# Performance work log

Hardware: AMD Instinct MI355X
Metric: run time of the kernel (lower is better)

Reference implementation:

```python
import jax, jax.numpy as jnp
import numpy as np

B, S, HID = 2, 2048, 2048
NH = 16
QLR, KVLR = 1536, 512
DN, DR, DV = 128, 64, 128          # qk_nope_head_dim, qk_rope_head_dim, v_head_dim
DQK = DN + DR                      # 192
SCALE = DQK ** -0.5
EPS = 1e-6


def rmsnorm(x, w):
    return x * jax.lax.rsqrt(jnp.mean(x * x, axis=-1, keepdims=True) + EPS) * w


def rotate_half(x):
    h = x.shape[-1] // 2
    return jnp.concatenate([-x[..., h:], x[..., :h]], axis=-1)


def setup_inputs() -> dict:
    key = jax.random.key(0)
    k = jax.random.split(key, 8)
    hidden_states = jax.random.normal(k[0], (B, S, HID), jnp.float32)
    # additive causal mask [B,1,S,S]
    causal = jnp.tril(jnp.ones((S, S), bool))
    attention_mask = jnp.where(causal, 0.0, -1e9).astype(jnp.float32)[None, None]
    attention_mask = jnp.broadcast_to(attention_mask, (B, 1, S, S))
    # RoPE tables for the rope head dim
    inv_freq = 1.0 / (10000.0 ** (jnp.arange(0, DR, 2, dtype=jnp.float32) / DR))
    t = jnp.arange(S, dtype=jnp.float32)[:, None] * inv_freq[None, :]
    emb = jnp.concatenate([t, t], axis=-1)        # [S, DR]
    cos, sin = jnp.cos(emb), jnp.sin(emb)
    s = 0.02
    w_qa = jax.random.normal(k[1], (HID, QLR), jnp.float32) * s
    qa_ln = jnp.ones((QLR,), jnp.float32)
    w_qb = jax.random.normal(k[2], (QLR, NH * DQK), jnp.float32) * s
    w_kva = jax.random.normal(k[3], (HID, KVLR + DR), jnp.float32) * s
    kva_ln = jnp.ones((KVLR,), jnp.float32)
    w_kvb = jax.random.normal(k[4], (KVLR, NH * (DN + DV)), jnp.float32) * s
    w_o = jax.random.normal(k[5], (NH * DV, HID), jnp.float32) * s
    return {"hidden_states": hidden_states, "attention_mask": attention_mask,
            "cos": cos, "sin": sin, "w_qa": w_qa, "qa_ln": qa_ln, "w_qb": w_qb,
            "w_kva": w_kva, "kva_ln": kva_ln, "w_kvb": w_kvb, "w_o": w_o}


def reference(hidden_states, attention_mask, cos, sin, w_qa, qa_ln, w_qb,
              w_kva, kva_ln, w_kvb, w_o):
    b, s, _ = hidden_states.shape
    # q low-rank path: q_b_proj(q_a_layernorm(q_a_proj(x)))
    q = rmsnorm(hidden_states @ w_qa, qa_ln) @ w_qb            # [B,S,NH*DQK]
    q = q.reshape(b, s, NH, DQK).transpose(0, 2, 1, 3)          # [B,NH,S,DQK]
    q_nope, q_pe = q[..., :DN], q[..., DN:]
    # compressed kv + shared rope key
    ckv = hidden_states @ w_kva                                 # [B,S,KVLR+DR]
    k_c, k_pe = ckv[..., :KVLR], ckv[..., KVLR:]
    kv = rmsnorm(k_c, kva_ln) @ w_kvb                           # [B,S,NH*(DN+DV)]
    kv = kv.reshape(b, s, NH, DN + DV).transpose(0, 2, 1, 3)    # [B,NH,S,DN+DV]
    k_nope, value_states = kv[..., :DN], kv[..., DN:]
    # RoPE on rope dims (k_pe is MQA: one head)
    k_pe = k_pe.reshape(b, 1, s, DR)
    c = cos[None, None]  # [1,1,S,DR]
    si = sin[None, None]
    q_pe = q_pe * c + rotate_half(q_pe) * si
    k_pe = k_pe * c + rotate_half(k_pe) * si
    k_pe = jnp.broadcast_to(k_pe, (b, NH, s, DR))
    query_states = jnp.concatenate([q_nope, q_pe], axis=-1)     # [B,NH,S,DQK]
    key_states = jnp.concatenate([k_nope, k_pe], axis=-1)       # [B,NH,S,DQK]
    attn_weights = jnp.einsum('bhqd,bhkd->bhqk', query_states, key_states) * SCALE
    attn_weights = attn_weights + attention_mask
    attn_probs = jax.nn.softmax(attn_weights.astype(jnp.float32), axis=-1)
    attn_probs = attn_probs.astype(value_states.dtype)
    attn_output = jnp.einsum('bhqk,bhkd->bhqd', attn_probs, value_states)
    attn_output = attn_output.transpose(0, 2, 1, 3).reshape(b, s, NH * DV)
    return attn_output @ w_o                                    # [B,S,HID]
```

## Files before the change

kernel.cpp:

```cpp
#include <hip/hip_runtime.h>
#include <type_traits>

typedef __attribute__((ext_vector_type(8))) short  vshort8;
typedef __attribute__((ext_vector_type(8))) __bf16 vbf16x8;
typedef __attribute__((ext_vector_type(4))) float  vfloat4;

__device__ __forceinline__ float bf2f(unsigned short h) {
    return __uint_as_float(((unsigned int)h) << 16);
}
__device__ __forceinline__ unsigned short f2bf(float f) {
    unsigned int u = __float_as_uint(f);
    unsigned int r = (u + 0x7FFFu + ((u >> 16) & 1u)) >> 16;
    return (unsigned short)r;
}
__device__ __forceinline__ vshort8 cvt8s(const float* p, float s) {
    float4 a = *(const float4*)p;
    float4 b = *(const float4*)(p + 4);
    vshort8 r;
    r[0] = (short)f2bf(a.x * s); r[1] = (short)f2bf(a.y * s);
    r[2] = (short)f2bf(a.z * s); r[3] = (short)f2bf(a.w * s);
    r[4] = (short)f2bf(b.x * s); r[5] = (short)f2bf(b.y * s);
    r[6] = (short)f2bf(b.z * s); r[7] = (short)f2bf(b.w * s);
    return r;
}
__device__ __forceinline__ vshort8 cvt8(const float* p) { return cvt8s(p, 1.0f); }
__device__ __forceinline__ void gload16(const void* g, void* lds) {
    __builtin_amdgcn_global_load_lds(
        (const __attribute__((address_space(1))) unsigned int*)g,
        (__attribute__((address_space(3))) unsigned int*)lds, 16, 0, 0);
}

__global__ __launch_bounds__(256) void hconv_kernel(
    const float* __restrict__ in, unsigned short* __restrict__ out, int n8)
{
    int i = blockIdx.x * 256 + threadIdx.x;
    if (i < n8) *(vshort8*)(out + (size_t)i * 8) = cvt8(in + (size_t)i * 8);
}

__global__ __launch_bounds__(256) void wtrans_kernel(
    const float* __restrict__ W, unsigned short* __restrict__ Wt,
    int ldw, int ldt, int rowoff, float scale)
{
    __shared__ __align__(16) unsigned short Ls[64][72];
    const int t = threadIdx.x;
    const int n0 = blockIdx.x * 64, k0 = blockIdx.y * 64;
    const int rr = t >> 2, cc = t & 3;

    const float* src = W + (size_t)(k0 + rr) * ldw + n0 + cc * 16;
    *(vshort8*)&Ls[rr][cc * 16]     = cvt8s(src, scale);
    *(vshort8*)&Ls[rr][cc * 16 + 8] = cvt8s(src + 8, scale);
    __syncthreads();

    unsigned short* dst = Wt + (size_t)(rowoff + n0 + rr) * ldt + k0 + cc * 16;
    vshort8 v0, v1;
    #pragma unroll
    for (int j = 0; j < 8; ++j) {
        v0[j] = (short)Ls[cc * 16 + j][rr];
        v1[j] = (short)Ls[cc * 16 + 8 + j][rr];
    }
    *(vshort8*)dst = v0;
    *(vshort8*)(dst + 8) = v1;
}

template<typename CT>
__global__ __launch_bounds__(256) void gemm_tt(
    const unsigned short* __restrict__ A, const unsigned short* __restrict__ Bt,
    CT* __restrict__ C0, CT* __restrict__ C1,
    int K, int N, int nsplit, int ldc0, int ldc1)
{
    __shared__ __align__(16) unsigned short As[128 * 32];
    __shared__ __align__(16) unsigned short Bs[128 * 32];

    const int t = threadIdx.x, lane = t & 63, w = t >> 6;
    const int lm = lane & 15, quad = lane >> 4;
    const int wm = w >> 1, wn = w & 1;
    const int m0 = blockIdx.y * 128, n0 = blockIdx.x * 128;
    const int srow = lane >> 2, sseg = lane & 3;

    vfloat4 acc[4][4] = {};

    for (int k0 = 0; k0 < K; k0 += 32) {
        #pragma unroll
        for (int j = 0; j < 2; ++j) {
            int r = w * 32 + j * 16 + srow;
            gload16(A  + (size_t)(m0 + r) * K + k0 + sseg * 8, &As[(w * 2 + j) * 512]);
            gload16(Bt + (size_t)(n0 + r) * K + k0 + sseg * 8, &Bs[(w * 2 + j) * 512]);
        }
        __syncthreads();

        vbf16x8 af[4], bw[4];
        #pragma unroll
        for (int i = 0; i < 4; ++i) {
            af[i] = *(const vbf16x8*)&As[(wm * 64 + i * 16 + lm) * 32 + quad * 8];
            bw[i] = *(const vbf16x8*)&Bs[(wn * 64 + i * 16 + lm) * 32 + quad * 8];
        }
        #pragma unroll
        for (int mi = 0; mi < 4; ++mi)
            #pragma unroll
            for (int ni = 0; ni < 4; ++ni)
                acc[mi][ni] = __builtin_amdgcn_mfma_f32_16x16x32_bf16(af[mi], bw[ni], acc[mi][ni], 0, 0, 0);
        __syncthreads();
    }

    #pragma unroll
    for (int mi = 0; mi < 4; ++mi) {
        #pragma unroll
        for (int ni = 0; ni < 4; ++ni) {
            int col = n0 + wn * 64 + ni * 16 + lm;
            if (col >= N) continue;
            #pragma unroll
            for (int r = 0; r < 4; ++r) {
                int row = m0 + wm * 64 + mi * 16 + quad * 4 + r;
                float v = acc[mi][ni][r];
                if (col < nsplit) {
                    if constexpr (std::is_same_v<CT, float>) C0[(size_t)row * ldc0 + col] = v;
                    else C0[(size_t)row * ldc0 + col] = f2bf(v);
                } else {
                    if constexpr (std::is_same_v<CT, float>) C1[(size_t)row * ldc1 + col - nsplit] = v;
                    else C1[(size_t)row * ldc1 + col - nsplit] = f2bf(v);
                }
            }
        }
    }
}

__global__ __launch_bounds__(256) void gemm_kv(
    const unsigned short* __restrict__ A, const unsigned short* __restrict__ Bt,
    unsigned short* __restrict__ Kn, unsigned short* __restrict__ VT, int K)
{
    __shared__ __align__(16) unsigned short As[128 * 32];
    __shared__ __align__(16) unsigned short Bs[128 * 32];

    const int t = threadIdx.x, lane = t & 63, w = t >> 6;
    const int lm = lane & 15, quad = lane >> 4;
    const int wm = w >> 1, wn = w & 1;
    const int m0 = blockIdx.y * 128, n0 = blockIdx.x * 128;
    const int srow = lane >> 2, sseg = lane & 3;

    vfloat4 acc[4][4] = {};

    for (int k0 = 0; k0 < K; k0 += 32) {
        #pragma unroll
        for (int j = 0; j < 2; ++j) {
            int r = w * 32 + j * 16 + srow;
            gload16(A  + (size_t)(m0 + r) * K + k0 + sseg * 8, &As[(w * 2 + j) * 512]);
            gload16(Bt + (size_t)(n0 + r) * K + k0 + sseg * 8, &Bs[(w * 2 + j) * 512]);
        }
        __syncthreads();

        vbf16x8 af[4], bw[4];
        #pragma unroll
        for (int i = 0; i < 4; ++i) {
            af[i] = *(const vbf16x8*)&As[(wm * 64 + i * 16 + lm) * 32 + quad * 8];
            bw[i] = *(const vbf16x8*)&Bs[(wn * 64 + i * 16 + lm) * 32 + quad * 8];
        }
        #pragma unroll
        for (int mi = 0; mi < 4; ++mi)
            #pragma unroll
            for (int ni = 0; ni < 4; ++ni)
                acc[mi][ni] = __builtin_amdgcn_mfma_f32_16x16x32_bf16(af[mi], bw[ni], acc[mi][ni], 0, 0, 0);
        __syncthreads();
    }

    #pragma unroll
    for (int mi = 0; mi < 4; ++mi) {
        #pragma unroll
        for (int ni = 0; ni < 4; ++ni) {
            int col = n0 + wn * 64 + ni * 16 + lm;
            int h = col >> 8, d = col & 255;
            #pragma unroll
            for (int r = 0; r < 4; ++r) {
                int row = m0 + wm * 64 + mi * 16 + quad * 4 + r;
                float v = acc[mi][ni][r];
                if (d < 128) {
                    Kn[(size_t)row * 2048 + h * 128 + d] = f2bf(v);
                } else {
                    int b = row >> 11, tok = row & 2047;
                    VT[((size_t)(b * 16 + h) * 128 + d - 128) * 2048 + tok] = f2bf(v);
                }
            }
        }
    }
}

__global__ __launch_bounds__(256) void rmsnorm_kernel(
    const unsigned short* __restrict__ in, const float* __restrict__ wgt,
    unsigned short* __restrict__ out, int width, int ld_in, int ld_out)
{
    const int row = blockIdx.x;
    const int t = threadIdx.x;
    const unsigned short* x = in + (size_t)row * ld_in;

    float ss = 0.f;
    for (int i = t; i < width; i += 256) { float v = bf2f(x[i]); ss += v * v; }
    #pragma unroll
    for (int off = 32; off > 0; off >>= 1) ss += __shfl_down(ss, off, 64);

    __shared__ float red[4];
    __shared__ float rr;
    if ((t & 63) == 0) red[t >> 6] = ss;
    __syncthreads();
    if (t == 0) rr = rsqrtf((red[0] + red[1] + red[2] + red[3]) / (float)width + 1e-6f);
    __syncthreads();
    float r = rr;
    unsigned short* o = out + (size_t)row * ld_out;
    for (int i = t; i < width; i += 256) o[i] = f2bf(bf2f(x[i]) * r * wgt[i]);
}

__global__ __launch_bounds__(256) void rope_q_kernel(
    unsigned short* __restrict__ q, const float* __restrict__ cosb,
    const float* __restrict__ sinb)
{
    const int row = blockIdx.x;
    const int s = row & 2047;
    const int t = threadIdx.x;
    unsigned short* qr = q + (size_t)row * 3072;
    const int i = t & 31;
    const float cs = cosb[s * 64 + i];
    const float sn = sinb[s * 64 + i];

    #pragma unroll
    for (int c = t; c < 512; c += 256) {
        int h = c >> 5;
        unsigned short* p = qr + h * 192 + 128 + i;
        float x = bf2f(p[0]);
        float y = bf2f(p[32]);
        p[0]  = f2bf(x * cs - y * sn);
        p[32] = f2bf(y * cs + x * sn);
    }
}

__global__ __launch_bounds__(64) void rope_k_kernel(
    const unsigned short* __restrict__ ckv, const float* __restrict__ cosb,
    const float* __restrict__ sinb, unsigned short* __restrict__ kpe)
{
    const int row = blockIdx.x;
    const int s = row & 2047;
    const int t = threadIdx.x;
    if (t < 32) {
        float cs = cosb[s * 64 + t];
        float sn = sinb[s * 64 + t];
        float x = bf2f(ckv[(size_t)row * 576 + 512 + t]);
        float y = bf2f(ckv[(size_t)row * 576 + 544 + t]);
        kpe[(size_t)row * 64 + t]      = f2bf(x * cs - y * sn);
        kpe[(size_t)row * 64 + 32 + t] = f2bf(y * cs + x * sn);
    }
}

__global__ __launch_bounds__(256) void flash_kernel(
    const unsigned short* __restrict__ Q, const unsigned short* __restrict__ Kn,
    const unsigned short* __restrict__ KPE, const unsigned short* __restrict__ VT,
    unsigned short* __restrict__ O)
{
    __shared__ __align__(16) unsigned short Ks[64][200];
    __shared__ __align__(16) unsigned short Vs[128][72];
    __shared__ __align__(16) unsigned short Ps[4][16][72];

    const int t    = threadIdx.x;
    const int lane = t & 63;
    const int w    = t >> 6;
    const int lm   = lane & 15, quad = lane >> 4;
    const int h = blockIdx.y, b = blockIdx.z;
    const int tb = b * 2048;
    const unsigned short* VTbh = VT + (size_t)(b * 16 + h) * 128 * 2048;

    for (int pi = 0; pi < 2; ++pi) {
        const int qt = pi ? (31 - blockIdx.x) : blockIdx.x;

        const int qtok = tb + qt * 64 + w * 16 + lm;
        vbf16x8 aq[6];
        #pragma unroll
        for (int ch = 0; ch < 6; ++ch)
            aq[ch] = *(const vbf16x8*)(Q + (size_t)qtok * 3072 + h * 192 + ch * 32 + quad * 8);

        vfloat4 acc_o[8];
        #pragma unroll
        for (int i = 0; i < 8; ++i) acc_o[i] = (vfloat4){0, 0, 0, 0};
        float mrow[4], lrow[4];
        #pragma unroll
        for (int r = 0; r < 4; ++r) { mrow[r] = -3.0e38f; lrow[r] = 0.f; }

        for (int kt = 0; kt <= qt; ++kt) {
            const int kb = kt * 64;
            #pragma unroll
            for (int it = 0; it < 4; ++it) {
                int idx = t + it * 256;
                int row = idx >> 4, sg = idx & 15;
                *(vshort8*)&Ks[row][sg * 8] =
                    *(const vshort8*)(Kn + (size_t)(tb + kb + row) * 2048 + h * 128 + sg * 8);
            }
            #pragma unroll
            for (int it = 0; it < 2; ++it) {
                int idx = t + it * 256;
                int row = idx >> 3, sg = idx & 7;
                *(vshort8*)&Ks[row][128 + sg * 8] =
                    *(const vshort8*)(KPE + (size_t)(tb + kb + row) * 64 + sg * 8);
            }
            #pragma unroll
            for (int it = 0; it < 4; ++it) {
                int idx = t + it * 256;
                int d = idx >> 3, sg = idx & 7;
                *(vshort8*)&Vs[d][sg * 8] =
                    *(const vshort8*)(VTbh + (size_t)d * 2048 + kb + sg * 8);
            }
            __syncthreads();

            vfloat4 accs[4];
            #pragma unroll
            for (int ni = 0; ni < 4; ++ni) accs[ni] = (vfloat4){0, 0, 0, 0};
            #pragma unroll
            for (int ni = 0; ni < 4; ++ni) {
                #pragma unroll
                for (int ch = 0; ch < 6; ++ch) {
                    vbf16x8 bk = *(const vbf16x8*)&Ks[ni * 16 + lm][ch * 32 + quad * 8];
                    accs[ni] = __builtin_amdgcn_mfma_f32_16x16x32_bf16(aq[ch], bk, accs[ni], 0, 0, 0);
                }
            }

            const int qrow = qt * 64 + w * 16 + quad * 4;
            #pragma unroll
            for (int ni = 0; ni < 4; ++ni) {
                int ki = kb + ni * 16 + lm;
                #pragma unroll
                for (int r = 0; r < 4; ++r)
                    if (ki > qrow + r) accs[ni][r] = -3.0e38f;
            }

            #pragma unroll
            for (int r = 0; r < 4; ++r) {
                float mx = fmaxf(fmaxf(accs[0][r], accs[1][r]), fmaxf(accs[2][r], accs[3][r]));
                #pragma unroll
                for (int off = 1; off < 16; off <<= 1) mx = fmaxf(mx, __shfl_xor(mx, off, 64));
                float mnew  = fmaxf(mrow[r], mx);
                float alpha = __expf(mrow[r] - mnew);
                float sum = 0.f;
                #pragma unroll
                for (int ni = 0; ni < 4; ++ni) {
                    float pv = __expf(accs[ni][r] - mnew);
                    accs[ni][r] = pv;
                    sum += pv;
                }
                #pragma unroll
                for (int off = 1; off < 16; off <<= 1) sum += __shfl_xor(sum, off, 64);
                lrow[r] = lrow[r] * alpha + sum;
                mrow[r] = mnew;
                #pragma unroll
                for (int vt = 0; vt < 8; ++vt) acc_o[vt][r] *= alpha;
            }

            #pragma unroll
            for (int ni = 0; ni < 4; ++ni)
                #pragma unroll
                for (int r = 0; r < 4; ++r)
                    Ps[w][quad * 4 + r][ni * 16 + lm] = f2bf(accs[ni][r]);
            __syncthreads();

            #pragma unroll
            for (int kc = 0; kc < 2; ++kc) {
                vbf16x8 ap = *(const vbf16x8*)&Ps[w][lm][kc * 32 + quad * 8];
                #pragma unroll
                for (int vt = 0; vt < 8; ++vt) {
                    vbf16x8 bv = *(const vbf16x8*)&Vs[vt * 16 + lm][kc * 32 + quad * 8];
                    acc_o[vt] = __builtin_amdgcn_mfma_f32_16x16x32_bf16(ap, bv, acc_o[vt], 0, 0, 0);
                }
            }
            __syncthreads();
        }

        #pragma unroll
        for (int r = 0; r < 4; ++r) {
            float inv = 1.f / lrow[r];
            int tok = tb + qt * 64 + w * 16 + quad * 4 + r;
            #pragma unroll
            for (int vt = 0; vt < 8; ++vt)
                O[(size_t)tok * 2048 + h * 128 + vt * 16 + lm] = f2bf(acc_o[vt][r] * inv);
        }
    }
}

extern "C" void kernel_launch(void* const* d_in, const int* in_sizes, int n_in,
                              void* d_out, int out_size, void* d_ws, size_t ws_size,
                              hipStream_t stream) {
    const float* hidden = (const float*)d_in[0];
    const float* cosb   = (const float*)d_in[2];
    const float* sinb   = (const float*)d_in[3];
    const float* w_qa   = (const float*)d_in[4];
    const float* qa_ln  = (const float*)d_in[5];
    const float* w_qb   = (const float*)d_in[6];
    const float* w_kva  = (const float*)d_in[7];
    const float* kva_ln = (const float*)d_in[8];
    const float* w_kvb  = (const float*)d_in[9];
    const float* w_o    = (const float*)d_in[10];
    float* out = (float*)d_out;
    const float SCALE = 0.07216878364870323f;

    unsigned short* ws   = (unsigned short*)d_ws;
    unsigned short* hb   = ws;
    unsigned short* Kn   = ws;
    unsigned short* wt12 = ws + 8388608;
    unsigned short* VT   = ws + 8388608;
    unsigned short* ot   = ws + 8388608;
    unsigned short* qbuf = ws + 16777216;
    unsigned short* q_a  = ws + 29360128;
    unsigned short* ckv  = ws + 35651584;
    unsigned short* aout = ws + 29360128;
    unsigned short* qbt  = ws + 38010880;
    unsigned short* kvbt = ws + 42729472;
    unsigned short* kvn  = ws + 44826624;
    unsigned short* kpe  = ws + 46923776;

    dim3 blk(256);

    hconv_kernel<<<4096, blk, 0, stream>>>(hidden, hb, 1048576);
    wtrans_kernel<<<dim3(24, 32), blk, 0, stream>>>(w_qa,  wt12, 1536, 2048, 0,    1.0f);
    wtrans_kernel<<<dim3( 9, 32), blk, 0, stream>>>(w_kva, wt12,  576, 2048, 1536, 1.0f);
    wtrans_kernel<<<dim3(48, 24), blk, 0, stream>>>(w_qb,  qbt,  3072, 1536, 0,    SCALE);
    wtrans_kernel<<<dim3(64,  8), blk, 0, stream>>>(w_kvb, kvbt, 4096,  512, 0,    1.0f);

    gemm_tt<unsigned short><<<dim3(17, 32), blk, 0, stream>>>(
        hb, wt12, q_a, ckv, 2048, 2112, 1536, 1536, 576);

    rmsnorm_kernel<<<4096, blk, 0, stream>>>(q_a, qa_ln, q_a, 1536, 1536, 1536);
    rmsnorm_kernel<<<4096, blk, 0, stream>>>(ckv, kva_ln, kvn, 512, 576, 512);
    rope_k_kernel<<<4096, dim3(64), 0, stream>>>(ckv, cosb, sinb, kpe);

    gemm_tt<unsigned short><<<dim3(24, 32), blk, 0, stream>>>(
        q_a, qbt, qbuf, qbuf, 1536, 3072, 3072, 3072, 3072);
    rope_q_kernel<<<4096, blk, 0, stream>>>(qbuf, cosb, sinb);

    gemm_kv<<<dim3(32, 32), blk, 0, stream>>>(kvn, kvbt, Kn, VT, 512);

    flash_kernel<<<dim3(16, 16, 2), blk, 0, stream>>>(qbuf, Kn, kpe, VT, aout);

    wtrans_kernel<<<dim3(32, 32), blk, 0, stream>>>(w_o, ot, 2048, 2048, 0, 1.0f);

    gemm_tt<float><<<dim3(16, 32), blk, 0, stream>>>(
        aout, ot, out, out, 2048, 2048, 2048, 2048, 2048);
}
```

Measured before the change: 546.1 us.

## Stage V transpose through LDS in gemm_kv and give flash one q-tile per block

The gemm_kv epilogue now splits by block column parity. K blocks write Kn directly, and V blocks stage their tile transposed in shared memory so that VT is written with coalesced 16-byte stores instead of scattered 2-byte writes. The flash kernel no longer pairs q-tiles inside each block. It launches 32x16x2 blocks, one q-tile each, ordered heaviest first, which doubles the number of blocks for better occupancy and gives up the explicit load balance of pairing. The extra shared-memory tile and barriers in gemm_kv add a little epilogue cost.

```diff
diff --git a/kernel.cpp b/kernel.cpp
--- a/kernel.cpp
+++ b/kernel.cpp
@@ -130,6 +130,7 @@
 {
     __shared__ __align__(16) unsigned short As[128 * 32];
     __shared__ __align__(16) unsigned short Bs[128 * 32];
+    __shared__ __align__(16) unsigned short Ts[64][136];
 
     const int t = threadIdx.x, lane = t & 63, w = t >> 6;
     const int lm = lane & 15, quad = lane >> 4;
@@ -162,23 +163,51 @@
         __syncthreads();
     }
 
-    #pragma unroll
-    for (int mi = 0; mi < 4; ++mi) {
-        #pragma unroll
-        for (int ni = 0; ni < 4; ++ni) {
-            int col = n0 + wn * 64 + ni * 16 + lm;
-            int h = col >> 8, d = col & 255;
-            #pragma unroll
-            for (int r = 0; r < 4; ++r) {
-                int row = m0 + wm * 64 + mi * 16 + quad * 4 + r;
-                float v = acc[mi][ni][r];
-                if (d < 128) {
-                    Kn[(size_t)row * 2048 + h * 128 + d] = f2bf(v);
-                } else {
-                    int b = row >> 11, tok = row & 2047;
-                    VT[((size_t)(b * 16 + h) * 128 + d - 128) * 2048 + tok] = f2bf(v);
+    if (!(blockIdx.x & 1)) {
+        const int hh = blockIdx.x >> 1;
+        #pragma unroll
+        for (int mi = 0; mi < 4; ++mi) {
+            #pragma unroll
+            for (int ni = 0; ni < 4; ++ni) {
+                int d = wn * 64 + ni * 16 + lm;
+                #pragma unroll
+                for (int r = 0; r < 4; ++r) {
+                    int row = m0 + wm * 64 + mi * 16 + quad * 4 + r;
+                    Kn[(size_t)row * 2048 + hh * 128 + d] = f2bf(acc[mi][ni][r]);
                 }
             }
+        }
+    } else {
+        const int hh   = blockIdx.x >> 1;
+        const int bb   = m0 >> 11;
+        const int tok0 = m0 & 2047;
+        #pragma unroll
+        for (int half = 0; half < 2; ++half) {
+            if (wn == half) {
+                #pragma unroll
+                for (int mi = 0; mi < 4; ++mi) {
+                    #pragma unroll
+                    for (int ni = 0; ni < 4; ++ni) {
+                        int ln = ni * 16 + lm;
+                        int rt = wm * 64 + mi * 16 + quad * 4;
+                        #pragma unroll
+                        for (int r = 0; r < 4; ++r)
+                            Ts[ln][rt + r] = f2bf(acc[mi][ni][r]);
+                    }
+                }
+            }
+            __syncthreads();
+            {
+                int tr = t >> 2, seg = t & 3;
+                int dv = half * 64 + tr;
+                unsigned short* dst =
+                    VT + ((size_t)(bb * 16 + hh) * 128 + dv) * 2048 + tok0 + seg * 32;
+                const unsigned short* srcp = &Ts[tr][seg * 32];
+                #pragma unroll
+                for (int j = 0; j < 4; ++j)
+                    *(vshort8*)(dst + j * 8) = *(const vshort8*)(srcp + j * 8);
+            }
+            __syncthreads();
         }
     }
 }
@@ -263,118 +292,115 @@
     const int h = blockIdx.y, b = blockIdx.z;
     const int tb = b * 2048;
     const unsigned short* VTbh = VT + (size_t)(b * 16 + h) * 128 * 2048;
-
-    for (int pi = 0; pi < 2; ++pi) {
-        const int qt = pi ? (31 - blockIdx.x) : blockIdx.x;
-
-        const int qtok = tb + qt * 64 + w * 16 + lm;
-        vbf16x8 aq[6];
-        #pragma unroll
-        for (int ch = 0; ch < 6; ++ch)
-            aq[ch] = *(const vbf16x8*)(Q + (size_t)qtok * 3072 + h * 192 + ch * 32 + quad * 8);
-
-        vfloat4 acc_o[8];
-        #pragma unroll
-        for (int i = 0; i < 8; ++i) acc_o[i] = (vfloat4){0, 0, 0, 0};
-        float mrow[4], lrow[4];
-        #pragma unroll
-        for (int r = 0; r < 4; ++r) { mrow[r] = -3.0e38f; lrow[r] = 0.f; }
-
-        for (int kt = 0; kt <= qt; ++kt) {
-            const int kb = kt * 64;
-            #pragma unroll
-            for (int it = 0; it < 4; ++it) {
-                int idx = t + it * 256;
-                int row = idx >> 4, sg = idx & 15;
-                *(vshort8*)&Ks[row][sg * 8] =
-                    *(const vshort8*)(Kn + (size_t)(tb + kb + row) * 2048 + h * 128 + sg * 8);
-            }
-            #pragma unroll
-            for (int it = 0; it < 2; ++it) {
-                int idx = t + it * 256;
-                int row = idx >> 3, sg = idx & 7;
-                *(vshort8*)&Ks[row][128 + sg * 8] =
-                    *(const vshort8*)(KPE + (size_t)(tb + kb + row) * 64 + sg * 8);
-            }
-            #pragma unroll
-            for (int it = 0; it < 4; ++it) {
-                int idx = t + it * 256;
-                int d = idx >> 3, sg = idx & 7;
-                *(vshort8*)&Vs[d][sg * 8] =
-                    *(const vshort8*)(VTbh + (size_t)d * 2048 + kb + sg * 8);
-            }
-            __syncthreads();
-
-            vfloat4 accs[4];
-            #pragma unroll
-            for (int ni = 0; ni < 4; ++ni) accs[ni] = (vfloat4){0, 0, 0, 0};
+    const int qt = 31 - (int)blockIdx.x;
+
+    const int qtok = tb + qt * 64 + w * 16 + lm;
+    vbf16x8 aq[6];
+    #pragma unroll
+    for (int ch = 0; ch < 6; ++ch)
+        aq[ch] = *(const vbf16x8*)(Q + (size_t)qtok * 3072 + h * 192 + ch * 32 + quad * 8);
+
+    vfloat4 acc_o[8];
+    #pragma unroll
+    for (int i = 0; i < 8; ++i) acc_o[i] = (vfloat4){0, 0, 0, 0};
+    float mrow[4], lrow[4];
+    #pragma unroll
+    for (int r = 0; r < 4; ++r) { mrow[r] = -3.0e38f; lrow[r] = 0.f; }
+
+    for (int kt = 0; kt <= qt; ++kt) {
+        const int kb = kt * 64;
+        #pragma unroll
+        for (int it = 0; it < 4; ++it) {
+            int idx = t + it * 256;
+            int row = idx >> 4, sg = idx & 15;
+            *(vshort8*)&Ks[row][sg * 8] =
+                *(const vshort8*)(Kn + (size_t)(tb + kb + row) * 2048 + h * 128 + sg * 8);
+        }
+        #pragma unroll
+        for (int it = 0; it < 2; ++it) {
+            int idx = t + it * 256;
+            int row = idx >> 3, sg = idx & 7;
+            *(vshort8*)&Ks[row][128 + sg * 8] =
+                *(const vshort8*)(KPE + (size_t)(tb + kb + row) * 64 + sg * 8);
+        }
+        #pragma unroll
+        for (int it = 0; it < 4; ++it) {
+            int idx = t + it * 256;
+            int d = idx >> 3, sg = idx & 7;
+            *(vshort8*)&Vs[d][sg * 8] =
+                *(const vshort8*)(VTbh + (size_t)d * 2048 + kb + sg * 8);
+        }
+        __syncthreads();
+
+        vfloat4 accs[4];
+        #pragma unroll
+        for (int ni = 0; ni < 4; ++ni) accs[ni] = (vfloat4){0, 0, 0, 0};
+        #pragma unroll
+        for (int ni = 0; ni < 4; ++ni) {
+            #pragma unroll
+            for (int ch = 0; ch < 6; ++ch) {
+                vbf16x8 bk = *(const vbf16x8*)&Ks[ni * 16 + lm][ch * 32 + quad * 8];
+                accs[ni] = __builtin_amdgcn_mfma_f32_16x16x32_bf16(aq[ch], bk, accs[ni], 0, 0, 0);
+            }
+        }
+
+        const int qrow = qt * 64 + w * 16 + quad * 4;
+        #pragma unroll
+        for (int ni = 0; ni < 4; ++ni) {
+            int ki = kb + ni * 16 + lm;
+            #pragma unroll
+            for (int r = 0; r < 4; ++r)
+                if (ki > qrow + r) accs[ni][r] = -3.0e38f;
+        }
+
+        #pragma unroll
+        for (int r = 0; r < 4; ++r) {
+            float mx = fmaxf(fmaxf(accs[0][r], accs[1][r]), fmaxf(accs[2][r], accs[3][r]));
+            #pragma unroll
+            for (int off = 1; off < 16; off <<= 1) mx = fmaxf(mx, __shfl_xor(mx, off, 64));
+            float mnew  = fmaxf(mrow[r], mx);
+            float alpha = __expf(mrow[r] - mnew);
+            float sum = 0.f;
             #pragma unroll
             for (int ni = 0; ni < 4; ++ni) {
-                #pragma unroll
-                for (int ch = 0; ch < 6; ++ch) {
-                    vbf16x8 bk = *(const vbf16x8*)&Ks[ni * 16 + lm][ch * 32 + quad * 8];
-                    accs[ni] = __builtin_amdgcn_mfma_f32_16x16x32_bf16(aq[ch], bk, accs[ni], 0, 0, 0);
-                }
-            }
-
-            const int qrow = qt * 64 + w * 16 + quad * 4;
-            #pragma unroll
-            for (int ni = 0; ni < 4; ++ni) {
-                int ki = kb + ni * 16 + lm;
-                #pragma unroll
-                for (int r = 0; r < 4; ++r)
-                    if (ki > qrow + r) accs[ni][r] = -3.0e38f;
-            }
-
-            #pragma unroll
-            for (int r = 0; r < 4; ++r) {
-                float mx = fmaxf(fmaxf(accs[0][r], accs[1][r]), fmaxf(accs[2][r], accs[3][r]));
-                #pragma unroll
-                for (int off = 1; off < 16; off <<= 1) mx = fmaxf(mx, __shfl_xor(mx, off, 64));
-                float mnew  = fmaxf(mrow[r], mx);
-                float alpha = __expf(mrow[r] - mnew);
-                float sum = 0.f;
-                #pragma unroll
-                for (int ni = 0; ni < 4; ++ni) {
-                    float pv = __expf(accs[ni][r] - mnew);
-                    accs[ni][r] = pv;
-                    sum += pv;
-                }
-                #pragma unroll
-                for (int off = 1; off < 16; off <<= 1) sum += __shfl_xor(sum, off, 64);
-                lrow[r] = lrow[r] * alpha + sum;
-                mrow[r] = mnew;
-                #pragma unroll
-                for (int vt = 0; vt < 8; ++vt) acc_o[vt][r] *= alpha;
-            }
-
-            #pragma unroll
-            for (int ni = 0; ni < 4; ++ni)
-                #pragma unroll
-                for (int r = 0; r < 4; ++r)
-                    Ps[w][quad * 4 + r][ni * 16 + lm] = f2bf(accs[ni][r]);
-            __syncthreads();
-
-            #pragma unroll
-            for (int kc = 0; kc < 2; ++kc) {
-                vbf16x8 ap = *(const vbf16x8*)&Ps[w][lm][kc * 32 + quad * 8];
-                #pragma unroll
-                for (int vt = 0; vt < 8; ++vt) {
-                    vbf16x8 bv = *(const vbf16x8*)&Vs[vt * 16 + lm][kc * 32 + quad * 8];
-                    acc_o[vt] = __builtin_amdgcn_mfma_f32_16x16x32_bf16(ap, bv, acc_o[vt], 0, 0, 0);
-                }
-            }
-            __syncthreads();
-        }
-
-        #pragma unroll
-        for (int r = 0; r < 4; ++r) {
-            float inv = 1.f / lrow[r];
-            int tok = tb + qt * 64 + w * 16 + quad * 4 + r;
-            #pragma unroll
-            for (int vt = 0; vt < 8; ++vt)
-                O[(size_t)tok * 2048 + h * 128 + vt * 16 + lm] = f2bf(acc_o[vt][r] * inv);
-        }
+                float pv = __expf(accs[ni][r] - mnew);
+                accs[ni][r] = pv;
+                sum += pv;
+            }
+            #pragma unroll
+            for (int off = 1; off < 16; off <<= 1) sum += __shfl_xor(sum, off, 64);
+            lrow[r] = lrow[r] * alpha + sum;
+            mrow[r] = mnew;
+            #pragma unroll
+            for (int vt = 0; vt < 8; ++vt) acc_o[vt][r] *= alpha;
+        }
+
+        #pragma unroll
+        for (int ni = 0; ni < 4; ++ni)
+            #pragma unroll
+            for (int r = 0; r < 4; ++r)
+                Ps[w][quad * 4 + r][ni * 16 + lm] = f2bf(accs[ni][r]);
+        __syncthreads();
+
+        #pragma unroll
+        for (int kc = 0; kc < 2; ++kc) {
+            vbf16x8 ap = *(const vbf16x8*)&Ps[w][lm][kc * 32 + quad * 8];
+            #pragma unroll
+            for (int vt = 0; vt < 8; ++vt) {
+                vbf16x8 bv = *(const vbf16x8*)&Vs[vt * 16 + lm][kc * 32 + quad * 8];
+                acc_o[vt] = __builtin_amdgcn_mfma_f32_16x16x32_bf16(ap, bv, acc_o[vt], 0, 0, 0);
+            }
+        }
+        __syncthreads();
+    }
+
+    #pragma unroll
+    for (int r = 0; r < 4; ++r) {
+        float inv = 1.f / lrow[r];
+        int tok = tb + qt * 64 + w * 16 + quad * 4 + r;
+        #pragma unroll
+        for (int vt = 0; vt < 8; ++vt)
+            O[(size_t)tok * 2048 + h * 128 + vt * 16 + lm] = f2bf(acc_o[vt][r] * inv);
     }
 }
 
@@ -430,7 +456,7 @@
 
     gemm_kv<<<dim3(32, 32), blk, 0, stream>>>(kvn, kvbt, Kn, VT, 512);
 
-    flash_kernel<<<dim3(16, 16, 2), blk, 0, stream>>>(qbuf, Kn, kpe, VT, aout);
+    flash_kernel<<<dim3(32, 16, 2), blk, 0, stream>>>(qbuf, Kn, kpe, VT, aout);
 
     wtrans_kernel<<<dim3(32, 32), blk, 0, stream>>>(w_o, ot, 2048, 2048, 0, 1.0f);
 
```

New measurement: 620.7 us. +13.7%, slower.
